# Kernel optimization log

Hardware: AMD Instinct MI355X
Metric: run time of the kernel (lower is better)

The kernel has to match this reference:

```python
import math
import jax, jax.numpy as jnp
import numpy as np

N_EMBD = 1024
N_HEAD = 16
HEAD_DIM = N_EMBD // N_HEAD


def setup_inputs() -> dict:
    key = jax.random.key(0)
    k1, k2, k3, k4, k5 = jax.random.split(key, 5)
    B, T, C = 1, 4096, N_EMBD
    s = 1.0 / math.sqrt(C)
    return {
        "x": jax.random.normal(k1, (B, T, C), dtype=jnp.float32),
        "w_qkv": jax.random.normal(k2, (C, 3 * C), dtype=jnp.float32) * s,
        "b_qkv": jnp.zeros((3 * C,), dtype=jnp.float32),
        "w_proj": jax.random.normal(k3, (C, C), dtype=jnp.float32) * s,
        "b_proj": jnp.zeros((C,), dtype=jnp.float32),
    }


def reference(x, w_qkv, b_qkv, w_proj, b_proj):
    B, T, C = x.shape
    qkv = x @ w_qkv + b_qkv                       # [B,T,3C]
    q, k, v = jnp.split(qkv, 3, axis=-1)
    # [B,T,C] -> [B,H,T,D]
    def heads(t):
        return t.reshape(B, T, N_HEAD, HEAD_DIM).transpose(0, 2, 1, 3)
    q, k, v = heads(q), heads(k), heads(v)
    scale = 1.0 / math.sqrt(HEAD_DIM)
    attn = jnp.einsum("bhqd,bhkd->bhqk", q, k) * scale
    causal = jnp.tril(jnp.ones((T, T), dtype=bool))
    attn = jnp.where(causal, attn, -jnp.inf)
    attn = jax.nn.softmax(attn, axis=-1)
    out = jnp.einsum("bhqk,bhkd->bhqd", attn, v)   # [B,H,T,D]
    out = out.transpose(0, 2, 1, 3).reshape(B, T, C)
    return out @ w_proj + b_proj
```

## Files before the change

### kernel.cpp

```cpp
#include <hip/hip_runtime.h>
#include <hip/hip_bf16.h>

#define TT 4096
#define CC 1024
#define NHEAD 16
#define DH 64
#define N3C 3072

typedef __attribute__((ext_vector_type(8))) short short8;
typedef __attribute__((ext_vector_type(4))) float floatx4;

#define QSCALE 0.18033688011112042f

__device__ __forceinline__ short f2bf(float f) {
    union { __hip_bfloat16 h; short s; } u;
    u.h = __float2bfloat16(f);
    return u.s;
}

__device__ __forceinline__ void gload_lds16(const void* g, void* l) {
    __builtin_amdgcn_global_load_lds(
        (const __attribute__((address_space(1))) unsigned int*)(unsigned long long)g,
        (__attribute__((address_space(3))) unsigned int*)(unsigned int)(unsigned long long)l,
        16, 0, 0);
}

__device__ __forceinline__ unsigned pk_trunc(float lo, float hi) {
    return __builtin_amdgcn_perm(__float_as_uint(hi), __float_as_uint(lo), 0x07060302u);
}

__device__ __forceinline__ void tr_body(const float* __restrict__ in, short* __restrict__ out,
                                        int K, int N, int bx, int by, int tid, float (*tile)[33]) {
    int nt = bx * 32, kt = by * 32;
    int tx = tid & 31, ty = tid >> 5;
#pragma unroll
    for (int i = 0; i < 32; i += 8)
        tile[ty + i][tx] = in[(size_t)(kt + ty + i) * N + nt + tx];
    __syncthreads();
#pragma unroll
    for (int i = 0; i < 32; i += 8)
        out[(size_t)(nt + ty + i) * K + kt + tx] = f2bf(tile[tx][ty + i]);
}

__global__ void k_prep(const float* __restrict__ x, short* __restrict__ xb,
                       const float* __restrict__ w_qkv, short* __restrict__ wqkvT,
                       const float* __restrict__ w_proj, short* __restrict__ wprojT) {
    __shared__ float tile[32][33];
    int id = blockIdx.x;
    int tid = threadIdx.x;
    if (id < 4096) {
        int i = (id * 256 + tid) * 4;
        float4 v = *(const float4*)&x[i];
        short4 r;
        r.x = f2bf(v.x); r.y = f2bf(v.y); r.z = f2bf(v.z); r.w = f2bf(v.w);
        *(short4*)&xb[i] = r;
    } else if (id < 4096 + 3072) {
        int r = id - 4096;
        tr_body(w_qkv, wqkvT, CC, N3C, r % 96, r / 96, tid, tile);
    } else {
        int r = id - 7168;
        tr_body(w_proj, wprojT, CC, CC, r & 31, r >> 5, tid, tile);
    }
}

__global__ __launch_bounds__(256) void k_gemm_qkv(const short* __restrict__ A,
                                                  const short* __restrict__ Bt,
                                                  const float* __restrict__ bias,
                                                  short* __restrict__ Q,
                                                  short* __restrict__ Kb,
                                                  short* __restrict__ Vtg) {
    const int m0 = blockIdx.y * 128;
    const int n0 = blockIdx.x * 128;
    __shared__ __attribute__((aligned(16))) short As[2][128 * 32];
    __shared__ __attribute__((aligned(16))) short Bs[2][128 * 32];
    const int tid = threadIdx.x;
    const int lane = tid & 63;
    const int w = tid >> 6;
    const int wm = w >> 1, wn = w & 1;
    const int quad = lane >> 4;
    const int l16 = lane & 15;

    const int r0 = tid >> 2, c0 = (tid & 3) * 8;
    const short* pA[2][2]; const short* pB[2][2];
    short* lA[2][2]; short* lB[2][2];
#pragma unroll
    for (int it = 0; it < 2; ++it)
#pragma unroll
        for (int hh = 0; hh < 2; ++hh) {
            pA[it][hh] = A + (size_t)(m0 + it * 64 + r0) * CC + hh * 32 + c0;
            pB[it][hh] = Bt + (size_t)(n0 + it * 64 + r0) * CC + hh * 32 + c0;
            lA[it][hh] = &As[hh][(it * 256 + w * 64) * 8];
            lB[it][hh] = &Bs[hh][(it * 256 + w * 64) * 8];
        }

    floatx4 acc[4][4] = {};
    for (int kb = 0; kb < CC; kb += 64) {
        __syncthreads();
#pragma unroll
        for (int it = 0; it < 2; ++it)
#pragma unroll
            for (int hh = 0; hh < 2; ++hh) {
                gload_lds16(pA[it][hh] + kb, lA[it][hh]);
                gload_lds16(pB[it][hh] + kb, lB[it][hh]);
            }
        __syncthreads();
#pragma unroll
        for (int kk = 0; kk < 2; ++kk) {
            short8 af[4], bf[4];
#pragma unroll
            for (int mi = 0; mi < 4; ++mi)
                af[mi] = *(const short8*)&As[kk][(wm * 64 + mi * 16 + l16) * 32 + quad * 8];
#pragma unroll
            for (int ni = 0; ni < 4; ++ni)
                bf[ni] = *(const short8*)&Bs[kk][(wn * 64 + ni * 16 + l16) * 32 + quad * 8];
#pragma unroll
            for (int mi = 0; mi < 4; ++mi)
#pragma unroll
                for (int ni = 0; ni < 4; ++ni)
                    acc[mi][ni] = __builtin_amdgcn_mfma_f32_16x16x32_bf16(af[mi], bf[ni], acc[mi][ni], 0, 0, 0);
        }
    }
#pragma unroll
    for (int mi = 0; mi < 4; ++mi) {
#pragma unroll
        for (int ni = 0; ni < 4; ++ni) {
            int gm = m0 + wm * 64 + mi * 16 + quad * 4;
            int gn = n0 + wn * 64 + ni * 16 + l16;
            int which = gn >> 10;
            int cc = gn & 1023;
            int h = cc >> 6, d = cc & 63;
            float bv = bias[gn];
            if (which == 0) {
#pragma unroll
                for (int r = 0; r < 4; ++r) {
                    float v = (acc[mi][ni][r] + bv) * QSCALE;
                    Q[((size_t)h * TT + (gm + r)) * DH + d] = f2bf(v);
                }
            } else if (which == 1) {
#pragma unroll
                for (int r = 0; r < 4; ++r) {
                    float v = acc[mi][ni][r] + bv;
                    Kb[((size_t)h * TT + (gm + r)) * DH + d] = f2bf(v);
                }
            } else {
                short4 vv;
                vv.x = f2bf(acc[mi][ni][0] + bv);
                vv.y = f2bf(acc[mi][ni][1] + bv);
                vv.z = f2bf(acc[mi][ni][2] + bv);
                vv.w = f2bf(acc[mi][ni][3] + bv);
                *(short4*)&Vtg[((size_t)h * DH + d) * TT + gm] = vv;
            }
        }
    }
}

__global__ __launch_bounds__(256) void k_attn(const short* __restrict__ Qh,
                                              const short* __restrict__ Kh,
                                              const short* __restrict__ VhT,
                                              short* __restrict__ Ob) {
    const int h = blockIdx.x;
    const int qi = 63 - blockIdx.y;
    const int tid = threadIdx.x, lane = tid & 63, w = tid >> 6;
    const int quad = lane >> 4, l16 = lane & 15;

    __shared__ __attribute__((aligned(16))) short Ps[2][64 * 136];
    __shared__ float wl[4][64];
    __shared__ float lsum[64];

    const short* Qp = Qh + (size_t)h * TT * DH;
    const short* Kp = Kh + (size_t)h * TT * DH;
    const short* Vp = VhT + (size_t)h * DH * TT;

    const int q0 = qi * 64;
    const int nk = (qi >> 1) + 1;

    short8 aq[4][2];
#pragma unroll
    for (int qg = 0; qg < 4; ++qg)
#pragma unroll
        for (int ss = 0; ss < 2; ++ss)
            aq[qg][ss] = *(const short8*)&Qp[(size_t)(q0 + qg * 16 + l16) * DH + ss * 32 + quad * 8];

    floatx4 accO[4] = {};
    float l_part[4] = {0.f, 0.f, 0.f, 0.f};
    int buf = 0;

    short8 kf[2][2];
#pragma unroll
    for (int mi = 0; mi < 2; ++mi)
#pragma unroll
        for (int ss = 0; ss < 2; ++ss)
            kf[mi][ss] = *(const short8*)&Kp[(size_t)(w * 32 + mi * 16 + l16) * DH + ss * 32 + quad * 8];

    for (int ki = 0; ki < nk; ++ki) {
        const int k0 = ki * 128;
        const bool masked = (ki == nk - 1);

        floatx4 accS[2][4] = {};
        __builtin_amdgcn_s_setprio(1);
#pragma unroll
        for (int mi = 0; mi < 2; ++mi)
#pragma unroll
            for (int ss = 0; ss < 2; ++ss)
#pragma unroll
                for (int qg = 0; qg < 4; ++qg)
                    accS[mi][qg] = __builtin_amdgcn_mfma_f32_16x16x32_bf16(kf[mi][ss], aq[qg][ss], accS[mi][qg], 0, 0, 0);
        __builtin_amdgcn_s_setprio(0);

        short* Pb = &Ps[buf][0];
#pragma unroll
        for (int mi = 0; mi < 2; ++mi) {
            const int kbase = k0 + w * 32 + mi * 16 + quad * 4;
#pragma unroll
            for (int qg = 0; qg < 4; ++qg) {
                float pv[4];
#pragma unroll
                for (int r = 0; r < 4; ++r) {
                    float e = __builtin_amdgcn_exp2f(accS[mi][qg][r]);
                    if (masked)
                        e = (kbase + r <= q0 + qg * 16 + l16) ? e : 0.f;
                    pv[r] = e;
                    l_part[qg] += e;
                }
                uint2 pk;
                pk.x = pk_trunc(pv[0], pv[1]);
                pk.y = pk_trunc(pv[2], pv[3]);
                *(uint2*)&Pb[(qg * 16 + l16) * 136 + w * 32 + mi * 16 + quad * 4] = pk;
            }
        }

        short8 vf[4];
#pragma unroll
        for (int ks = 0; ks < 4; ++ks)
            vf[ks] = *(const short8*)&Vp[(size_t)(w * 16 + l16) * TT + k0 + ks * 32 + quad * 8];

        short8 kfn[2][2];
        if (ki + 1 < nk) {
            const int kn0 = k0 + 128;
#pragma unroll
            for (int mi = 0; mi < 2; ++mi)
#pragma unroll
                for (int ss = 0; ss < 2; ++ss)
                    kfn[mi][ss] = *(const short8*)&Kp[(size_t)(kn0 + w * 32 + mi * 16 + l16) * DH + ss * 32 + quad * 8];
        }

        asm volatile("s_waitcnt lgkmcnt(0)" ::: "memory");
        __builtin_amdgcn_s_barrier();
        asm volatile("" ::: "memory");

        __builtin_amdgcn_s_setprio(1);
#pragma unroll
        for (int qg = 0; qg < 4; ++qg)
#pragma unroll
            for (int ks = 0; ks < 4; ++ks) {
                short8 ap = *(const short8*)&Pb[(qg * 16 + l16) * 136 + ks * 32 + quad * 8];
                accO[qg] = __builtin_amdgcn_mfma_f32_16x16x32_bf16(ap, vf[ks], accO[qg], 0, 0, 0);
            }
        __builtin_amdgcn_s_setprio(0);

#pragma unroll
        for (int mi = 0; mi < 2; ++mi)
#pragma unroll
            for (int ss = 0; ss < 2; ++ss)
                kf[mi][ss] = kfn[mi][ss];
        buf ^= 1;
    }

#pragma unroll
    for (int qg = 0; qg < 4; ++qg) {
        float lr = l_part[qg];
        lr += __shfl_xor(lr, 16, 64);
        lr += __shfl_xor(lr, 32, 64);
        if (lane < 16) wl[w][qg * 16 + lane] = lr;
    }
    __syncthreads();
    if (tid < 64) lsum[tid] = wl[0][tid] + wl[1][tid] + wl[2][tid] + wl[3][tid];
    __syncthreads();

#pragma unroll
    for (int qg = 0; qg < 4; ++qg) {
#pragma unroll
        for (int r = 0; r < 4; ++r) {
            int q = qg * 16 + quad * 4 + r;
            float o = accO[qg][r] / lsum[q];
            Ob[(size_t)(q0 + q) * CC + h * DH + w * 16 + l16] = f2bf(o);
        }
    }
}

__global__ __launch_bounds__(256) void k_gemm_proj(const short* __restrict__ A,
                                                   const short* __restrict__ Bt,
                                                   const float* __restrict__ bias,
                                                   float* __restrict__ out) {
    const int m0 = blockIdx.y * 128;
    const int n0 = blockIdx.x * 128;
    __shared__ __attribute__((aligned(16))) short As[2][128 * 32];
    __shared__ __attribute__((aligned(16))) short Bs[2][128 * 32];
    const int tid = threadIdx.x;
    const int lane = tid & 63;
    const int w = tid >> 6;
    const int wm = w >> 1, wn = w & 1;
    const int quad = lane >> 4;
    const int l16 = lane & 15;

    const int r0 = tid >> 2, c0 = (tid & 3) * 8;
    const short* pA[2][2]; const short* pB[2][2];
    short* lA[2][2]; short* lB[2][2];
#pragma unroll
    for (int it = 0; it < 2; ++it)
#pragma unroll
        for (int hh = 0; hh < 2; ++hh) {
            pA[it][hh] = A + (size_t)(m0 + it * 64 + r0) * CC + hh * 32 + c0;
            pB[it][hh] = Bt + (size_t)(n0 + it * 64 + r0) * CC + hh * 32 + c0;
            lA[it][hh] = &As[hh][(it * 256 + w * 64) * 8];
            lB[it][hh] = &Bs[hh][(it * 256 + w * 64) * 8];
        }

    floatx4 acc[4][4] = {};
    for (int kb = 0; kb < CC; kb += 64) {
        __syncthreads();
#pragma unroll
        for (int it = 0; it < 2; ++it)
#pragma unroll
            for (int hh = 0; hh < 2; ++hh) {
                gload_lds16(pA[it][hh] + kb, lA[it][hh]);
                gload_lds16(pB[it][hh] + kb, lB[it][hh]);
            }
        __syncthreads();
#pragma unroll
        for (int kk = 0; kk < 2; ++kk) {
            short8 af[4], bf[4];
#pragma unroll
            for (int mi = 0; mi < 4; ++mi)
                af[mi] = *(const short8*)&As[kk][(wm * 64 + mi * 16 + l16) * 32 + quad * 8];
#pragma unroll
            for (int ni = 0; ni < 4; ++ni)
                bf[ni] = *(const short8*)&Bs[kk][(wn * 64 + ni * 16 + l16) * 32 + quad * 8];
#pragma unroll
            for (int mi = 0; mi < 4; ++mi)
#pragma unroll
                for (int ni = 0; ni < 4; ++ni)
                    acc[mi][ni] = __builtin_amdgcn_mfma_f32_16x16x32_bf16(af[mi], bf[ni], acc[mi][ni], 0, 0, 0);
        }
    }
#pragma unroll
    for (int mi = 0; mi < 4; ++mi) {
#pragma unroll
        for (int ni = 0; ni < 4; ++ni) {
            int gm = m0 + wm * 64 + mi * 16 + quad * 4;
            int gn = n0 + wn * 64 + ni * 16 + l16;
            float bv = bias[gn];
#pragma unroll
            for (int r = 0; r < 4; ++r)
                out[(size_t)(gm + r) * CC + gn] = acc[mi][ni][r] + bv;
        }
    }
}

extern "C" void kernel_launch(void* const* d_in, const int* in_sizes, int n_in,
                              void* d_out, int out_size, void* d_ws, size_t ws_size,
                              hipStream_t stream) {
    const float* x      = (const float*)d_in[0];
    const float* w_qkv  = (const float*)d_in[1];
    const float* b_qkv  = (const float*)d_in[2];
    const float* w_proj = (const float*)d_in[3];
    const float* b_proj = (const float*)d_in[4];
    float* out = (float*)d_out;
    char* ws = (char*)d_ws;

    short* xb     = (short*)(ws);
    short* wqkvT  = (short*)(ws + 8388608);
    short* wprojT = (short*)(ws + 14680064);
    short* Qh     = (short*)(ws + 16777216);
    short* Kh     = (short*)(ws + 25165824);
    short* VhT    = (short*)(ws + 33554432);
    short* Ob     = (short*)(ws + 41943040);

    k_prep<<<8192, 256, 0, stream>>>(x, xb, w_qkv, wqkvT, w_proj, wprojT);
    k_gemm_qkv<<<dim3(N3C / 128, TT / 128), 256, 0, stream>>>(xb, wqkvT, b_qkv, Qh, Kh, VhT);
    k_attn<<<dim3(NHEAD, 64), 256, 0, stream>>>(Qh, Kh, VhT, Ob);
    k_gemm_proj<<<dim3(CC / 128, TT / 128), 256, 0, stream>>>(Ob, wprojT, b_proj, out);
}
```

Before: 213.4 us.

## Split long causal query tiles across two blocks and merge with combine kernel

The attention kernel now divides the key range of the 24 longest query tiles per head between two blocks. Each half writes unnormalized fp32 partial outputs and row sums to workspace, and a new combine kernel adds the halves and normalizes them into the bf16 output. Shorter tiles still run in a single block. The aim is to even out the per-block work imbalance of causal attention and shorten the tail. The cost is an extra kernel launch and extra partial-result traffic, stored in workspace regions reused from buffers that are already consumed.

Result: slower. 228.3 us (+6.9%).

```diff
diff --git a/kernel.cpp b/kernel.cpp
--- a/kernel.cpp
+++ b/kernel.cpp
@@ -157,9 +157,28 @@
 __global__ __launch_bounds__(256) void k_attn(const short* __restrict__ Qh,
                                               const short* __restrict__ Kh,
                                               const short* __restrict__ VhT,
-                                              short* __restrict__ Ob) {
+                                              short* __restrict__ Ob,
+                                              float* __restrict__ Opart,
+                                              float* __restrict__ Lpart) {
     const int h = blockIdx.x;
-    const int qi = 63 - blockIdx.y;
+    const int y = blockIdx.y;
+    int qi, kbeg, kend, pid;
+    if (y < 48) {
+        qi = 63 - (y >> 1);
+        const int nkt = (qi >> 1) + 1;
+        const int nh = (nkt + 1) >> 1;
+        const int half = y & 1;
+        kbeg = half ? nh : 0;
+        kend = half ? nkt : nh;
+        pid = ((h * 24) + (63 - qi)) * 2 + half;
+    } else {
+        qi = 87 - y;
+        kbeg = 0;
+        kend = (qi >> 1) + 1;
+        pid = -1;
+    }
+    const int nk = (qi >> 1) + 1;
+
     const int tid = threadIdx.x, lane = tid & 63, w = tid >> 6;
     const int quad = lane >> 4, l16 = lane & 15;
 
@@ -172,7 +191,6 @@
     const short* Vp = VhT + (size_t)h * DH * TT;
 
     const int q0 = qi * 64;
-    const int nk = (qi >> 1) + 1;
 
     short8 aq[4][2];
 #pragma unroll
@@ -190,9 +208,9 @@
     for (int mi = 0; mi < 2; ++mi)
 #pragma unroll
         for (int ss = 0; ss < 2; ++ss)
-            kf[mi][ss] = *(const short8*)&Kp[(size_t)(w * 32 + mi * 16 + l16) * DH + ss * 32 + quad * 8];
-
-    for (int ki = 0; ki < nk; ++ki) {
+            kf[mi][ss] = *(const short8*)&Kp[(size_t)(kbeg * 128 + w * 32 + mi * 16 + l16) * DH + ss * 32 + quad * 8];
+
+    for (int ki = kbeg; ki < kend; ++ki) {
         const int k0 = ki * 128;
         const bool masked = (ki == nk - 1);
 
@@ -235,7 +253,7 @@
             vf[ks] = *(const short8*)&Vp[(size_t)(w * 16 + l16) * TT + k0 + ks * 32 + quad * 8];
 
         short8 kfn[2][2];
-        if (ki + 1 < nk) {
+        if (ki + 1 < kend) {
             const int kn0 = k0 + 128;
 #pragma unroll
             for (int mi = 0; mi < 2; ++mi)
@@ -277,14 +295,57 @@
     if (tid < 64) lsum[tid] = wl[0][tid] + wl[1][tid] + wl[2][tid] + wl[3][tid];
     __syncthreads();
 
-#pragma unroll
-    for (int qg = 0; qg < 4; ++qg) {
-#pragma unroll
-        for (int r = 0; r < 4; ++r) {
-            int q = qg * 16 + quad * 4 + r;
-            float o = accO[qg][r] / lsum[q];
-            Ob[(size_t)(q0 + q) * CC + h * DH + w * 16 + l16] = f2bf(o);
-        }
+    if (pid >= 0) {
+        float* Op = Opart + (size_t)pid * 4096;
+#pragma unroll
+        for (int qg = 0; qg < 4; ++qg) {
+#pragma unroll
+            for (int r = 0; r < 4; ++r) {
+                int q = qg * 16 + quad * 4 + r;
+                Op[q * 64 + w * 16 + l16] = accO[qg][r];
+            }
+        }
+        if (tid < 64) Lpart[pid * 64 + tid] = lsum[tid];
+    } else {
+#pragma unroll
+        for (int qg = 0; qg < 4; ++qg) {
+#pragma unroll
+            for (int r = 0; r < 4; ++r) {
+                int q = qg * 16 + quad * 4 + r;
+                float o = accO[qg][r] / lsum[q];
+                Ob[(size_t)(q0 + q) * CC + h * DH + w * 16 + l16] = f2bf(o);
+            }
+        }
+    }
+}
+
+__global__ __launch_bounds__(256) void k_comb(const float* __restrict__ Opart,
+                                              const float* __restrict__ Lpart,
+                                              short* __restrict__ Ob) {
+    const int h = blockIdx.x;
+    const int t = blockIdx.y;
+    const int qi = 63 - t;
+    const int q0 = qi * 64;
+    const int p0 = ((h * 24) + t) * 2;
+    const float* O0 = Opart + (size_t)p0 * 4096;
+    const float* O1 = O0 + 4096;
+    const float* L0 = Lpart + p0 * 64;
+    const float* L1 = L0 + 64;
+    const int tid = threadIdx.x;
+    const int base = tid * 16;
+    const int q = base >> 6;
+    const float inv = 1.f / (L0[q] + L1[q]);
+    short* ob = Ob + (size_t)(q0 + q) * CC + h * DH + (base & 63);
+#pragma unroll
+    for (int i = 0; i < 16; i += 4) {
+        float4 a = *(const float4*)&O0[base + i];
+        float4 b = *(const float4*)&O1[base + i];
+        short4 r;
+        r.x = f2bf((a.x + b.x) * inv);
+        r.y = f2bf((a.y + b.y) * inv);
+        r.z = f2bf((a.z + b.z) * inv);
+        r.w = f2bf((a.w + b.w) * inv);
+        *(short4*)&ob[i] = r;
     }
 }
 
@@ -376,8 +437,12 @@
     short* VhT    = (short*)(ws + 33554432);
     short* Ob     = (short*)(ws + 41943040);
 
+    float* Opart = (float*)(ws);
+    float* Lpart = (float*)(ws + 12582912);
+
     k_prep<<<8192, 256, 0, stream>>>(x, xb, w_qkv, wqkvT, w_proj, wprojT);
     k_gemm_qkv<<<dim3(N3C / 128, TT / 128), 256, 0, stream>>>(xb, wqkvT, b_qkv, Qh, Kh, VhT);
-    k_attn<<<dim3(NHEAD, 64), 256, 0, stream>>>(Qh, Kh, VhT, Ob);
+    k_attn<<<dim3(NHEAD, 88), 256, 0, stream>>>(Qh, Kh, VhT, Ob, Opart, Lpart);
+    k_comb<<<dim3(NHEAD, 24), 256, 0, stream>>>(Opart, Lpart, Ob);
     k_gemm_proj<<<dim3(CC / 128, TT / 128), 256, 0, stream>>>(Ob, wprojT, b_proj, out);
 }
```
